# Kernel optimization log

Hardware: AMD Instinct MI355X
Metric: run time of the kernel (lower is better)

Reference implementation:

```python
import jax, jax.numpy as jnp
import numpy as np

# static config (matches torch module instantiation)
B, D, NH, HD = 2, 256, 8, 32
NL, NP, DFF = 1, 4, 1024
SHAPES = [(180, 180)]          # (H, W) per level; 180*180 = 32400
STARTS = [0]
LSRC = 32400
N_DET, N_SEG = 200, 100        # SEG_QUERY_NUM=100 -> num_seg_query=300
LQ = N_DET + N_SEG


def _lin(key, dout, din, scale=None):
    scale = scale if scale is not None else 1.0 / np.sqrt(din)
    k1, k2 = jax.random.split(key)
    return (jax.random.normal(k1, (dout, din), jnp.float32) * scale,
            jax.random.normal(k2, (dout,), jnp.float32) * 0.01)


def setup_inputs() -> dict:
    key = jax.random.key(0)
    ks = iter(jax.random.split(key, 64))
    inp = {
        'query': jax.random.normal(next(ks), (B, LQ, D), jnp.float32),
        'query_pos': jax.random.normal(next(ks), (B, LQ, D), jnp.float32),
        'src': jax.random.normal(next(ks), (B, LSRC, D), jnp.float32),
        'pos': jax.random.normal(next(ks), (B, LSRC, D), jnp.float32),
        'reference_points': jax.random.uniform(next(ks), (B, LSRC + LQ, NL, 2), jnp.float32),
        'spatial_shapes': jnp.array(SHAPES, jnp.int32),
        'level_start_index': jnp.array(STARTS, jnp.int32),
    }
    # two MSDeformAttn instances (self_attn = sa_*, cross_attn = ca_*)
    for pre in ('sa', 'ca'):
        inp[pre + '_Wv'], inp[pre + '_bv'] = _lin(next(ks), D, D)
        inp[pre + '_Woff'], inp[pre + '_boff'] = _lin(next(ks), NH * NL * NP * 2, D, scale=0.01)
        inp[pre + '_Waw'], inp[pre + '_baw'] = _lin(next(ks), NH * NL * NP, D, scale=0.01)
        inp[pre + '_Wout'], inp[pre + '_bout'] = _lin(next(ks), D, D)
    for nm in ('norm1', 'norm2', 'normq', 'qa_norm', 'norm3'):
        inp[nm + '_g'] = jnp.ones((D,), jnp.float32)
        inp[nm + '_b'] = jnp.zeros((D,), jnp.float32)
    inp['ffn1_W1'], inp['ffn1_b1'] = _lin(next(ks), DFF, D)
    inp['ffn1_W2'], inp['ffn1_b2'] = _lin(next(ks), D, DFF)
    inp['ffn3_W1'], inp['ffn3_b1'] = _lin(next(ks), DFF, D)
    inp['ffn3_W2'], inp['ffn3_b2'] = _lin(next(ks), D, DFF)
    # TCSLayer: proj(d->2d) then gate1/gate2 (d->d), sigmoid gates
    inp['tcs_Wp'], inp['tcs_bp'] = _lin(next(ks), 2 * D, D)
    inp['tcs_Wg1'], inp['tcs_bg1'] = _lin(next(ks), D, D)
    inp['tcs_Wg2'], inp['tcs_bg2'] = _lin(next(ks), D, D)
    # query self-attention (nn.MultiheadAttention): packed in_proj [3D, D]
    inp['qa_Win'], inp['qa_bin'] = _lin(next(ks), 3 * D, D)
    inp['qa_Wout'], inp['qa_bout'] = _lin(next(ks), D, D)
    return inp


def ln(x, g, b, eps=1e-5):
    m = x.mean(-1, keepdims=True)
    v = ((x - m) ** 2).mean(-1, keepdims=True)
    return (x - m) * jax.lax.rsqrt(v + eps) * g + b


def msda(q, ref, src_v, Wv, bv, Woff, boff, Waw, baw, Wout, bout):
    """MSDeformAttn: value proj -> learned offsets/weights -> bilinear sample -> out proj.
    q [B,Lq,D], ref [B,Lq,NL,2] in [0,1], src_v [B,Lin,D]."""
    Bq, Lq, _ = q.shape
    Lin = src_v.shape[1]
    value = (src_v @ Wv.T + bv).reshape(Bq, Lin, NH, HD).transpose(0, 2, 1, 3)  # [B,NH,Lin,HD]
    off = (q @ Woff.T + boff).reshape(Bq, Lq, NH, NL, NP, 2)
    aw = jax.nn.softmax((q @ Waw.T + baw).reshape(Bq, Lq, NH, NL * NP), -1)
    aw = aw.reshape(Bq, Lq, NH, NL, NP)
    norm = jnp.array([[w, h] for (h, w) in SHAPES], q.dtype)  # [NL,2] = (W,H)
    loc = ref[:, :, None, :, None, :] + off / norm[None, None, None, :, None, :]
    out = jnp.zeros((Bq, NH, Lq, HD), q.dtype)
    for l, (h, w) in enumerate(SHAPES):
        s = STARTS[l]
        v_l = value[:, :, s:s + h * w, :]
        # grid_sample align_corners=False: pixel = loc*size - 0.5, zero padding
        x = loc[:, :, :, l, :, 0] * w - 0.5  # [B,Lq,NH,NP]
        y = loc[:, :, :, l, :, 1] * h - 0.5
        x0 = jnp.floor(x); y0 = jnp.floor(y)
        lx = x - x0; ly = y - y0
        x0i = x0.astype(jnp.int32); y0i = y0.astype(jnp.int32)
        samp = jnp.zeros((Bq, NH, Lq, NP, HD), q.dtype)
        for dy, dx, wgt in ((0, 0, (1 - lx) * (1 - ly)), (0, 1, lx * (1 - ly)),
                            (1, 0, (1 - lx) * ly), (1, 1, lx * ly)):
            xi = x0i + dx; yi = y0i + dy
            valid = ((xi >= 0) & (xi < w) & (yi >= 0) & (yi < h)).astype(q.dtype)
            idx = jnp.clip(yi, 0, h - 1) * w + jnp.clip(xi, 0, w - 1)  # [B,Lq,NH,NP]
            idx_t = idx.transpose(0, 2, 1, 3).reshape(Bq, NH, Lq * NP)
            g = jnp.take_along_axis(v_l, idx_t[..., None], axis=2).reshape(Bq, NH, Lq, NP, HD)
            samp = samp + g * (wgt * valid).transpose(0, 2, 1, 3)[..., None]
        out = out + jnp.einsum('bhqpd,bqhp->bhqd', samp, aw[:, :, :, l, :])
    out = out.transpose(0, 2, 1, 3).reshape(Bq, Lq, NH * HD)
    return out @ Wout.T + bout


def mha(x, pos, Win, bin_, Wout, bout):
    qk = x + pos
    q = (qk @ Win[:D].T + bin_[:D]).reshape(*x.shape[:2], NH, HD)
    k = (qk @ Win[D:2 * D].T + bin_[D:2 * D]).reshape(*x.shape[:2], NH, HD)
    v = (x @ Win[2 * D:].T + bin_[2 * D:]).reshape(*x.shape[:2], NH, HD)
    attn = jax.nn.softmax(jnp.einsum('bqhd,bkhd->bhqk', q, k) / np.sqrt(HD), -1)
    o = jnp.einsum('bhqk,bkhd->bqhd', attn, v).reshape(*x.shape[:2], D)
    return o @ Wout.T + bout


def reference(query, query_pos, src, pos, reference_points, spatial_shapes, level_start_index,
              sa_Wv, sa_bv, sa_Woff, sa_boff, sa_Waw, sa_baw, sa_Wout, sa_bout,
              ca_Wv, ca_bv, ca_Woff, ca_boff, ca_Waw, ca_baw, ca_Wout, ca_bout,
              norm1_g, norm1_b, norm2_g, norm2_b, normq_g, normq_b,
              qa_norm_g, qa_norm_b, norm3_g, norm3_b,
              ffn1_W1, ffn1_b1, ffn1_W2, ffn1_b2,
              ffn3_W1, ffn3_b1, ffn3_W2, ffn3_b2,
              tcs_Wp, tcs_bp, tcs_Wg1, tcs_bg1, tcs_Wg2, tcs_bg2,
              qa_Win, qa_bin, qa_Wout, qa_bout):
    # deformable self-attn over BEV tokens
    src2 = msda(src + pos, reference_points[:, :LSRC], src,
                sa_Wv, sa_bv, sa_Woff, sa_boff, sa_Waw, sa_baw, sa_Wout, sa_bout)
    src = ln(src + src2, norm1_g, norm1_b)
    # FFN 1
    h = jax.nn.relu(src @ ffn1_W1.T + ffn1_b1) @ ffn1_W2.T + ffn1_b2
    src = ln(src + h, norm2_g, norm2_b)
    # TCS gating (USE_SIGMOID_GATE, not SPLIT_GATE, no OCC)
    gd, gs = jnp.split(jax.nn.gelu(src @ tcs_Wp.T + tcs_bp, approximate=False), 2, axis=-1)
    gate_det = jax.nn.sigmoid(gd @ tcs_Wg1.T + tcs_bg1)
    gate_seg = jax.nn.sigmoid(gs @ tcs_Wg2.T + tcs_bg2)
    # gated deformable cross-attn (shared cross_attn weights)
    q_det = msda(query[:, :N_DET] + query_pos[:, :N_DET],
                 reference_points[:, LSRC:LSRC + N_DET], src * gate_det,
                 ca_Wv, ca_bv, ca_Woff, ca_boff, ca_Waw, ca_baw, ca_Wout, ca_bout)
    q_seg = msda(query[:, N_DET:LQ] + query_pos[:, N_DET:LQ],
                 reference_points[:, LSRC + N_DET:LSRC + LQ], src * gate_seg,
                 ca_Wv, ca_bv, ca_Woff, ca_boff, ca_Waw, ca_baw, ca_Wout, ca_bout)
    query2 = jnp.concatenate([q_det, q_seg], 1)
    query = ln(query + query2, normq_g, normq_b)
    # query self-attention (post-norm)
    query = ln(query + mha(query, query_pos, qa_Win, qa_bin, qa_Wout, qa_bout),
               qa_norm_g, qa_norm_b)
    # FFN 3
    h3 = jax.nn.relu(query @ ffn3_W1.T + ffn3_b1) @ ffn3_W2.T + ffn3_b2
    query = ln(query + h3, norm3_g, norm3_b)
    return (query, src, gate_det, gate_seg)
```

## Files before the change

kernel.cpp:

```cpp
#include <hip/hip_runtime.h>
#include <hip/hip_bf16.h>
#include <cmath>

using bf16 = __hip_bfloat16;
typedef __bf16 bf16x8 __attribute__((ext_vector_type(8)));
typedef __bf16 bf16x4 __attribute__((ext_vector_type(4)));
typedef float f32x4 __attribute__((ext_vector_type(4)));

constexpr int D = 256;
constexpr int LSRC = 32400;
constexpr int NB = 2;
constexpr int LQ = 300;
constexpr int NDET = 200;
constexpr int MS = NB * LSRC;
constexpr int MQ = NB * LQ;
constexpr int RP_STRIDE = LSRC + LQ;
constexpr float IMGW = 180.f, IMGH = 180.f;
constexpr int IW = 180, IH = 180;

constexpr long long OFF_Q  = 0;
constexpr long long OFF_S  = (long long)MQ * D;
constexpr long long OFF_GD = OFF_S + (long long)MS * D;
constexpr long long OFF_GS = OFF_GD + (long long)MS * D;

__device__ inline void gload16(const void* g, void* l) {
  __builtin_amdgcn_global_load_lds(
      (const __attribute__((address_space(1))) void*)g,
      (__attribute__((address_space(3))) void*)l, 16, 0, 0);
}

__device__ inline int xcd_swz(int b, int nwg) {
  int q = nwg >> 3, r = nwg & 7;
  int xcd = b & 7, i = b >> 3;
  return (xcd < r ? xcd * (q + 1) : r * (q + 1) + (xcd - r) * q) + i;
}

__global__ void detect_kernel(const void* g, int* flag) {
  *flag = (*(const unsigned*)g == 0x3F803F80u) ? 1 : 0;
}

struct CvtEnt { const void* src; void* dst; int n; int f32out; };
struct CvtBatch { CvtEnt e[48]; int blk0[49]; int cnt; };

__global__ __launch_bounds__(256) void cvt_batch_kernel(CvtBatch cb, const int* __restrict__ flag) {
  int bid = blockIdx.x;
  int i = 0;
  for (int j = 1; j < cb.cnt; ++j) if (cb.blk0[j] <= bid) i = j;
  const CvtEnt en = cb.e[i];
  int idx = (bid - cb.blk0[i]) * 2048 + threadIdx.x * 8;
  if (idx >= en.n) return;
  const bool isb = (*flag != 0);
  if (en.f32out) {
    float v[8];
    if (isb) {
      bf16x8 x = *(const bf16x8*)((const __bf16*)en.src + idx);
#pragma unroll
      for (int j = 0; j < 8; ++j) v[j] = (float)x[j];
    } else {
      const float* s = (const float*)en.src + idx;
#pragma unroll
      for (int j = 0; j < 8; ++j) v[j] = s[j];
    }
    float* o = (float*)en.dst + idx;
#pragma unroll
    for (int j = 0; j < 8; ++j) o[j] = v[j];
  } else {
    if (isb) {
      uint4 x = *(const uint4*)((const char*)en.src + (size_t)idx * 2);
      *(uint4*)((char*)en.dst + (size_t)idx * 2) = x;
    } else {
      const float* s = (const float*)en.src + idx;
      bf16x8 o;
#pragma unroll
      for (int j = 0; j < 8; ++j) o[j] = (__bf16)s[j];
      *(bf16x8*)((__bf16*)en.dst + idx) = o;
    }
  }
}

__global__ __launch_bounds__(256) void cvt_add(const void* __restrict__ a, const void* __restrict__ b,
                                               const int* __restrict__ flag,
                                               bf16* __restrict__ a_b, bf16* __restrict__ b_b,
                                               bf16* __restrict__ sum, int n8) {
  int i = blockIdx.x * 256 + threadIdx.x;
  if (i >= n8) return;
  const bool isb = (*flag != 0);
  float va[8], vb[8];
  bf16x8 ab, bb;
  if (isb) {
    ab = *(const bf16x8*)((const __bf16*)a + (size_t)i * 8);
    bb = *(const bf16x8*)((const __bf16*)b + (size_t)i * 8);
#pragma unroll
    for (int j = 0; j < 8; ++j) { va[j] = (float)ab[j]; vb[j] = (float)bb[j]; }
  } else {
    const float* pa = (const float*)a + (size_t)i * 8;
    const float* pb = (const float*)b + (size_t)i * 8;
#pragma unroll
    for (int j = 0; j < 8; ++j) { va[j] = pa[j]; vb[j] = pb[j]; ab[j] = (__bf16)va[j]; bb[j] = (__bf16)vb[j]; }
  }
  bf16x8 sb;
#pragma unroll
  for (int j = 0; j < 8; ++j) sb[j] = (__bf16)(va[j] + vb[j]);
  if (a_b) *(bf16x8*)((__bf16*)a_b + (size_t)i * 8) = ab;
  if (b_b) *(bf16x8*)((__bf16*)b_b + (size_t)i * 8) = bb;
  *(bf16x8*)((__bf16*)sum + (size_t)i * 8) = sb;
}

__global__ __launch_bounds__(256) void add8(const bf16* __restrict__ a, const bf16* __restrict__ b,
                                            bf16* __restrict__ o, int n8) {
  int i = blockIdx.x * 256 + threadIdx.x;
  if (i >= n8) return;
  bf16x8 va = *(const bf16x8*)((const __bf16*)a + (size_t)i * 8);
  bf16x8 vb = *(const bf16x8*)((const __bf16*)b + (size_t)i * 8);
  bf16x8 vo;
#pragma unroll
  for (int j = 0; j < 8; ++j) vo[j] = (__bf16)((float)va[j] + (float)vb[j]);
  *(bf16x8*)((__bf16*)o + (size_t)i * 8) = vo;
}

template<int ACT, int OUTB, int RESM>
__global__ __launch_bounds__(256) void gemm_bt(
    const bf16* __restrict__ A, int lda,
    const bf16* __restrict__ Wt,
    const bf16* __restrict__ bias,
    const void* __restrict__ res,
    void* __restrict__ out, int ldo,
    int M, int N, int K)
{
  __shared__ __bf16 As[2][64 * 32];
  __shared__ __bf16 Bs[2][64 * 32];
  const int gy = gridDim.y;
  const int nwg = gridDim.x * gy;
  const int t = xcd_swz(blockIdx.y * gridDim.x + blockIdx.x, nwg);
  const int m0 = (t / gy) * 64;
  const int n0 = (t % gy) * 64;
  const int tid = threadIdx.x;
  const int lane = tid & 63, wid = tid >> 6;
  const int wm = (wid >> 1) * 32, wn = (wid & 1) * 32;
  f32x4 acc[2][2] = {};
  const int lr = tid >> 2;
  const int lc = (tid & 3) * 8;
  const bf16* Ap = A + (size_t)(m0 + lr) * lda + lc;
  const bf16* Wp = Wt + (size_t)(n0 + lr) * K + lc;
  const int fr = lane & 15, ks = (lane >> 4) * 8;

  for (int k0 = 0; k0 < K; k0 += 64) {
    __syncthreads();
#pragma unroll
    for (int kk = 0; kk < 2; ++kk) {
      const int kc = k0 + kk * 32;
      gload16((const __bf16*)Ap + kc, &As[kk][8 * tid]);
      gload16((const __bf16*)Wp + kc, &Bs[kk][8 * tid]);
    }
    __syncthreads();
#pragma unroll
    for (int kk = 0; kk < 2; ++kk) {
      bf16x8 a0 = *(const bf16x8*)&As[kk][(wm + fr) * 32 + ks];
      bf16x8 a1 = *(const bf16x8*)&As[kk][(wm + 16 + fr) * 32 + ks];
      bf16x8 b0 = *(const bf16x8*)&Bs[kk][(wn + fr) * 32 + ks];
      bf16x8 b1 = *(const bf16x8*)&Bs[kk][(wn + 16 + fr) * 32 + ks];
      acc[0][0] = __builtin_amdgcn_mfma_f32_16x16x32_bf16(a0, b0, acc[0][0], 0, 0, 0);
      acc[0][1] = __builtin_amdgcn_mfma_f32_16x16x32_bf16(a0, b1, acc[0][1], 0, 0, 0);
      acc[1][0] = __builtin_amdgcn_mfma_f32_16x16x32_bf16(a1, b0, acc[1][0], 0, 0, 0);
      acc[1][1] = __builtin_amdgcn_mfma_f32_16x16x32_bf16(a1, b1, acc[1][1], 0, 0, 0);
    }
  }

  const int rq = (lane >> 4) * 4;
#pragma unroll
  for (int fm = 0; fm < 2; ++fm)
#pragma unroll
  for (int fn = 0; fn < 2; ++fn) {
    int ncol = n0 + wn + fn * 16 + fr;
    if (ncol >= N) continue;
    float bvs = (float)bias[ncol];
#pragma unroll
    for (int i = 0; i < 4; ++i) {
      int mrow = m0 + wm + fm * 16 + rq + i;
      if (mrow >= M) continue;
      float v = acc[fm][fn][i] + bvs;
      if (RESM == 1) v += (float)((const bf16*)res)[(size_t)mrow * ldo + ncol];
      else if (RESM == 2) v += ((const float*)res)[(size_t)mrow * ldo + ncol];
      if (ACT == 1) v = fmaxf(v, 0.f);
      else if (ACT == 2) v = 0.5f * v * (1.f + erff(v * 0.7071067811865476f));
      else if (ACT == 3) v = 1.f / (1.f + __expf(-v));
      if (OUTB) ((bf16*)out)[(size_t)mrow * ldo + ncol] = (bf16)v;
      else ((float*)out)[(size_t)mrow * ldo + ncol] = v;
    }
  }
}

template<int ACT, int OUTB, int RESM, int EMIT>
__global__ __launch_bounds__(256) void gemm128(
    const bf16* __restrict__ A, int lda,
    const bf16* __restrict__ Wt,
    const bf16* __restrict__ bias,
    const void* __restrict__ res,
    void* __restrict__ out, int ldo,
    int M, int N, int K,
    const int* __restrict__ flagp, void* __restrict__ ob, long long eoff)
{
  __shared__ __bf16 As[2][128 * 32];
  __shared__ __bf16 Bs[2][128 * 32];
  const int gy = gridDim.y;
  const int nwg = gridDim.x * gy;
  const int t = xcd_swz(blockIdx.y * gridDim.x + blockIdx.x, nwg);
  const int m0 = (t / gy) * 128;
  const int n0 = (t % gy) * 128;
  const int tid = threadIdx.x;
  const int lane = tid & 63, wid = tid >> 6;
  const int wr = (wid >> 1) * 64, wc = (wid & 1) * 64;
  const int fr = lane & 15, ks = (lane >> 4) * 8;
  f32x4 acc[4][4] = {};

  const int srow = tid >> 2;
  const int scol = (tid & 3) * 8;
  const bf16* Ap0 = A + (size_t)(m0 + srow) * lda + scol;
  const bf16* Ap1 = A + (size_t)(m0 + 64 + srow) * lda + scol;
  const bf16* Bp0 = Wt + (size_t)(n0 + srow) * K + scol;
  const bf16* Bp1 = Wt + (size_t)(n0 + 64 + srow) * K + scol;

  for (int k0 = 0; k0 < K; k0 += 64) {
    __syncthreads();
#pragma unroll
    for (int kk = 0; kk < 2; ++kk) {
      const int kc = k0 + kk * 32;
      gload16((const __bf16*)Ap0 + kc, &As[kk][8 * tid]);
      gload16((const __bf16*)Ap1 + kc, &As[kk][64 * 32 + 8 * tid]);
      gload16((const __bf16*)Bp0 + kc, &Bs[kk][8 * tid]);
      gload16((const __bf16*)Bp1 + kc, &Bs[kk][64 * 32 + 8 * tid]);
    }
    __syncthreads();
#pragma unroll
    for (int kk = 0; kk < 2; ++kk) {
      bf16x8 af[4], bfv[4];
#pragma unroll
      for (int m = 0; m < 4; ++m) af[m]  = *(const bf16x8*)&As[kk][(wr + m * 16 + fr) * 32 + ks];
#pragma unroll
      for (int n = 0; n < 4; ++n) bfv[n] = *(const bf16x8*)&Bs[kk][(wc + n * 16 + fr) * 32 + ks];
#pragma unroll
      for (int m = 0; m < 4; ++m)
#pragma unroll
        for (int n = 0; n < 4; ++n)
          acc[m][n] = __builtin_amdgcn_mfma_f32_16x16x32_bf16(af[m], bfv[n], acc[m][n], 0, 0, 0);
    }
  }

  const bool isb = EMIT ? (*flagp != 0) : false;
  const int rq = (lane >> 4) * 4;
#pragma unroll
  for (int m = 0; m < 4; ++m) {
    const int mb = m0 + wr + m * 16 + rq;
#pragma unroll
    for (int n = 0; n < 4; ++n) {
      const int ncol = n0 + wc + n * 16 + fr;
      const float bvs = (float)bias[ncol];
#pragma unroll
      for (int i = 0; i < 4; ++i) {
        const int mrow = mb + i;
        if (mrow >= M) continue;
        float v = acc[m][n][i] + bvs;
        if (RESM == 1) v += (float)((const bf16*)res)[(size_t)mrow * ldo + ncol];
        else if (RESM == 2) v += ((const float*)res)[(size_t)mrow * ldo + ncol];
        if (ACT == 1) v = fmaxf(v, 0.f);
        else if (ACT == 2) v = 0.5f * v * (1.f + erff(v * 0.7071067811865476f));
        else if (ACT == 3) v = 1.f / (1.f + __expf(-v));
        if (OUTB) ((bf16*)out)[(size_t)mrow * ldo + ncol] = (bf16)v;
        else ((float*)out)[(size_t)mrow * ldo + ncol] = v;
        if (EMIT) {
          long long eo = eoff + (long long)mrow * ldo + ncol;
          if (isb) ((__bf16*)ob)[eo] = (__bf16)v;
          else ((float*)ob)[eo] = v;
        }
      }
    }
  }
}

__global__ __launch_bounds__(256) void gemm_gated(
    const bf16* __restrict__ S, const bf16* __restrict__ G, int lda,
    const bf16* __restrict__ Wt,
    const bf16* __restrict__ bias,
    bf16* __restrict__ out, int ldo,
    int M, int N, int K)
{
  __shared__ __bf16 As[2][128 * 32];
  __shared__ __bf16 Bs[2][128 * 32];
  const int gy = gridDim.y;
  const int nwg = gridDim.x * gy;
  const int t = xcd_swz(blockIdx.y * gridDim.x + blockIdx.x, nwg);
  const int m0 = (t / gy) * 128;
  const int n0 = (t % gy) * 128;
  const int tid = threadIdx.x;
  const int lane = tid & 63, wid = tid >> 6;
  const int wr = (wid >> 1) * 64, wc = (wid & 1) * 64;
  const int fr = lane & 15, ks = (lane >> 4) * 8;
  f32x4 acc[4][4] = {};

  const int srow = tid >> 2;
  const int scol = (tid & 3) * 8;
  const bf16* Sp0 = S + (size_t)(m0 + srow) * lda + scol;
  const bf16* Sp1 = S + (size_t)(m0 + 64 + srow) * lda + scol;
  const bf16* Gp0 = G + (size_t)(m0 + srow) * lda + scol;
  const bf16* Gp1 = G + (size_t)(m0 + 64 + srow) * lda + scol;
  const bf16* Bp0 = Wt + (size_t)(n0 + srow) * K + scol;
  const bf16* Bp1 = Wt + (size_t)(n0 + 64 + srow) * K + scol;

  for (int k0 = 0; k0 < K; k0 += 64) {
    bf16x8 a0[2], a1[2];
#pragma unroll
    for (int kk = 0; kk < 2; ++kk) {
      const int kc = k0 + kk * 32;
      bf16x8 s0 = *(const bf16x8*)((const __bf16*)Sp0 + kc);
      bf16x8 g0 = *(const bf16x8*)((const __bf16*)Gp0 + kc);
      bf16x8 s1 = *(const bf16x8*)((const __bf16*)Sp1 + kc);
      bf16x8 g1 = *(const bf16x8*)((const __bf16*)Gp1 + kc);
#pragma unroll
      for (int j = 0; j < 8; ++j) {
        a0[kk][j] = (__bf16)((float)s0[j] * (float)g0[j]);
        a1[kk][j] = (__bf16)((float)s1[j] * (float)g1[j]);
      }
    }
    __syncthreads();
#pragma unroll
    for (int kk = 0; kk < 2; ++kk) {
      const int kc = k0 + kk * 32;
      *(bf16x8*)&As[kk][8 * tid] = a0[kk];
      *(bf16x8*)&As[kk][64 * 32 + 8 * tid] = a1[kk];
      gload16((const __bf16*)Bp0 + kc, &Bs[kk][8 * tid]);
      gload16((const __bf16*)Bp1 + kc, &Bs[kk][64 * 32 + 8 * tid]);
    }
    __syncthreads();
#pragma unroll
    for (int kk = 0; kk < 2; ++kk) {
      bf16x8 af[4], bfv[4];
#pragma unroll
      for (int m = 0; m < 4; ++m) af[m]  = *(const bf16x8*)&As[kk][(wr + m * 16 + fr) * 32 + ks];
#pragma unroll
      for (int n = 0; n < 4; ++n) bfv[n] = *(const bf16x8*)&Bs[kk][(wc + n * 16 + fr) * 32 + ks];
#pragma unroll
      for (int m = 0; m < 4; ++m)
#pragma unroll
        for (int n = 0; n < 4; ++n)
          acc[m][n] = __builtin_amdgcn_mfma_f32_16x16x32_bf16(af[m], bfv[n], acc[m][n], 0, 0, 0);
    }
  }

  const int rq = (lane >> 4) * 4;
#pragma unroll
  for (int m = 0; m < 4; ++m) {
    const int mb = m0 + wr + m * 16 + rq;
#pragma unroll
    for (int n = 0; n < 4; ++n) {
      const int ncol = n0 + wc + n * 16 + fr;
      const float bvs = (float)bias[ncol];
#pragma unroll
      for (int i = 0; i < 4; ++i) {
        const int mrow = mb + i;
        if (mrow >= M) continue;
        out[(size_t)mrow * ldo + ncol] = (bf16)(acc[m][n][i] + bvs);
      }
    }
  }
}

template<int RESM, int EMIT, int OUTF>
__global__ __launch_bounds__(256) void gemm_ln(
    const bf16* __restrict__ A, int lda,
    const bf16* __restrict__ Wt,
    const bf16* __restrict__ bias,
    const void* __restrict__ res,
    const bf16* __restrict__ g, const bf16* __restrict__ b,
    bf16* __restrict__ outb, float* __restrict__ outf,
    int M, int K,
    const int* __restrict__ flagp, void* __restrict__ ob, long long eoff)
{
  __shared__ __bf16 As[2][64 * 32];
  __shared__ __bf16 Bs[2][256 * 32];
  __shared__ float redS[4][64], redQ[4][64];
  const int m0 = blockIdx.x * 64;
  const int tid = threadIdx.x, lane = tid & 63, wid = tid >> 6;
  const int wc = wid * 64;
  const int fr = lane & 15, ks = (lane >> 4) * 8;
  f32x4 acc[4][4] = {};
  const int srow = tid >> 2, scol = (tid & 3) * 8;
  const bf16* Ap = A + (size_t)(m0 + srow) * lda + scol;
  const bf16* Bp = Wt + (size_t)srow * K + scol;

  for (int k0 = 0; k0 < K; k0 += 64) {
    __syncthreads();
#pragma unroll
    for (int kk = 0; kk < 2; ++kk) {
      const int kc = k0 + kk * 32;
      gload16((const __bf16*)Ap + kc, &As[kk][8 * tid]);
#pragma unroll
      for (int j = 0; j < 4; ++j)
        gload16((const __bf16*)(Bp + (size_t)j * 64 * K) + kc, &Bs[kk][j * 64 * 32 + 8 * tid]);
    }
    __syncthreads();
#pragma unroll
    for (int kk = 0; kk < 2; ++kk) {
      bf16x8 af[4], bfv[4];
#pragma unroll
      for (int m = 0; m < 4; ++m) af[m]  = *(const bf16x8*)&As[kk][(m * 16 + fr) * 32 + ks];
#pragma unroll
      for (int n = 0; n < 4; ++n) bfv[n] = *(const bf16x8*)&Bs[kk][(wc + n * 16 + fr) * 32 + ks];
#pragma unroll
      for (int m = 0; m < 4; ++m)
#pragma unroll
        for (int n = 0; n < 4; ++n)
          acc[m][n] = __builtin_amdgcn_mfma_f32_16x16x32_bf16(af[m], bfv[n], acc[m][n], 0, 0, 0);
    }
  }

  const int rq = (lane >> 4) * 4;
  float bvals[4], gvals[4], bb2[4];
#pragma unroll
  for (int n = 0; n < 4; ++n) {
    bvals[n] = (float)bias[wc + n * 16 + fr];
    gvals[n] = (float)g[wc + n * 16 + fr];
    bb2[n]   = (float)b[wc + n * 16 + fr];
  }
#pragma unroll
  for (int m = 0; m < 4; ++m)
#pragma unroll
  for (int i = 0; i < 4; ++i) {
    const int mrow = m0 + m * 16 + rq + i;
#pragma unroll
    for (int n = 0; n < 4; ++n) {
      float r;
      if (RESM == 1) r = (float)((const bf16*)res)[(size_t)mrow * 256 + wc + n * 16 + fr];
      else           r = ((const float*)res)[(size_t)mrow * 256 + wc + n * 16 + fr];
      acc[m][n][i] += bvals[n] + r;
    }
    float s = acc[m][0][i] + acc[m][1][i] + acc[m][2][i] + acc[m][3][i];
    float q = acc[m][0][i] * acc[m][0][i] + acc[m][1][i] * acc[m][1][i]
            + acc[m][2][i] * acc[m][2][i] + acc[m][3][i] * acc[m][3][i];
#pragma unroll
    for (int off = 1; off <= 8; off <<= 1) {
      s += __shfl_xor(s, off);
      q += __shfl_xor(q, off);
    }
    if (fr == 0) { redS[wid][m * 16 + rq + i] = s; redQ[wid][m * 16 + rq + i] = q; }
  }
  __syncthreads();
  const bool isb = EMIT ? (*flagp != 0) : false;
#pragma unroll
  for (int m = 0; m < 4; ++m)
#pragma unroll
  for (int i = 0; i < 4; ++i) {
    const int rl = m * 16 + rq + i;
    const int mrow = m0 + rl;
    if (mrow >= M) continue;
    float ts = redS[0][rl] + redS[1][rl] + redS[2][rl] + redS[3][rl];
    float tq = redQ[0][rl] + redQ[1][rl] + redQ[2][rl] + redQ[3][rl];
    float mean = ts * (1.f / 256.f);
    float var = tq * (1.f / 256.f) - mean * mean;
    float rstd = rsqrtf(var + 1e-5f);
#pragma unroll
    for (int n = 0; n < 4; ++n) {
      const int col = wc + n * 16 + fr;
      float y = (acc[m][n][i] - mean) * rstd * gvals[n] + bb2[n];
      if (outb) outb[(size_t)mrow * 256 + col] = (bf16)y;
      if (OUTF) outf[(size_t)mrow * 256 + col] = y;
      if (EMIT) {
        long long eo = eoff + (long long)mrow * 256 + col;
        if (isb) ((__bf16*)ob)[eo] = (__bf16)y;
        else ((float*)ob)[eo] = y;
      }
    }
  }
}

__global__ __launch_bounds__(256) void msda_sample4(
    const float* __restrict__ oa,
    const float* __restrict__ rpf, int rp_base, int qi0, int qcnt4, int lqrow,
    const bf16* __restrict__ val, bf16* __restrict__ out) {
  int blk = blockIdx.x;
  int b = blk / qcnt4;
  int wid = threadIdx.x >> 6, lane = threadIdx.x & 63;
  int qi = qi0 + (blk % qcnt4) * 4 + wid;
  size_t row = (size_t)b * lqrow + qi;
  int h = lane >> 3, d0 = (lane & 7) * 4;
  const __bf16* vb = (const __bf16*)val + (size_t)b * LSRC * 256 + h * 32 + d0;
  float rx = rpf[((size_t)b * RP_STRIDE + rp_base + qi) * 2 + 0];
  float ry = rpf[((size_t)b * RP_STRIDE + rp_base + qi) * 2 + 1];
  const float* offp = oa + row * 96 + h * 8;
  const float* awp  = oa + row * 96 + 64 + h * 4;
  float a0 = awp[0], a1 = awp[1], a2 = awp[2], a3 = awp[3];
  float mx = fmaxf(fmaxf(a0, a1), fmaxf(a2, a3));
  float e0 = __expf(a0 - mx), e1 = __expf(a1 - mx), e2 = __expf(a2 - mx), e3 = __expf(a3 - mx);
  float rs = 1.f / (e0 + e1 + e2 + e3);
  float aws[4] = { e0 * rs, e1 * rs, e2 * rs, e3 * rs };
  float o0 = 0.f, o1 = 0.f, o2 = 0.f, o3 = 0.f;
#pragma unroll
  for (int p = 0; p < 4; ++p) {
    float x = rx * IMGW + offp[p * 2 + 0] - 0.5f;
    float y = ry * IMGH + offp[p * 2 + 1] - 0.5f;
    float x0f = floorf(x), y0f = floorf(y);
    float lx = x - x0f, ly = y - y0f;
    int x0 = (int)x0f, y0 = (int)y0f;
#pragma unroll
    for (int dy = 0; dy < 2; ++dy)
#pragma unroll
    for (int dx = 0; dx < 2; ++dx) {
      int xi = x0 + dx, yi = y0 + dy;
      if (xi >= 0 && xi < IW && yi >= 0 && yi < IH) {
        float wgt = aws[p] * (dx ? lx : 1.f - lx) * (dy ? ly : 1.f - ly);
        bf16x4 gv = *(const bf16x4*)(vb + (size_t)(yi * IW + xi) * 256);
        o0 += wgt * (float)gv[0]; o1 += wgt * (float)gv[1];
        o2 += wgt * (float)gv[2]; o3 += wgt * (float)gv[3];
      }
    }
  }
  bf16x4 ov;
  ov[0] = (__bf16)o0; ov[1] = (__bf16)o1; ov[2] = (__bf16)o2; ov[3] = (__bf16)o3;
  *(bf16x4*)((__bf16*)out + row * 256 + h * 32 + d0) = ov;
}

__global__ __launch_bounds__(256) void mha_attn(
    const float* __restrict__ qk,
    const float* __restrict__ v,
    bf16* __restrict__ o) {
  __shared__ float probs[4][304];
  int bh = blockIdx.x / 75;
  int j  = blockIdx.x % 75;
  int b = bh >> 3, h = bh & 7;
  int wid = threadIdx.x >> 6, lane = threadIdx.x & 63;
  const float scale = 0.17677669529663687f;
  int q = j * 4 + wid;
  const float* qv = qk + ((size_t)(b * 300 + q)) * 512 + h * 32;
  float p[5];
  float mx = -1e30f;
#pragma unroll
  for (int s5 = 0; s5 < 5; ++s5) {
    int k = lane + 64 * s5;
    float sacc = -1e30f;
    if (k < 300) {
      const float* kv = qk + ((size_t)(b * 300 + k)) * 512 + 256 + h * 32;
      float sd = 0.f;
#pragma unroll
      for (int dd = 0; dd < 32; ++dd) sd += qv[dd] * kv[dd];
      sacc = sd * scale;
    }
    p[s5] = sacc;
    mx = fmaxf(mx, sacc);
  }
#pragma unroll
  for (int off = 32; off; off >>= 1) mx = fmaxf(mx, __shfl_xor(mx, off));
  float ssum = 0.f;
#pragma unroll
  for (int s5 = 0; s5 < 5; ++s5) {
    p[s5] = (p[s5] > -1e29f) ? __expf(p[s5] - mx) : 0.f;
    ssum += p[s5];
  }
#pragma unroll
  for (int off = 32; off; off >>= 1) ssum += __shfl_xor(ssum, off);
  float rinv = 1.f / ssum;
#pragma unroll
  for (int s5 = 0; s5 < 5; ++s5) {
    int k = lane + 64 * s5;
    if (k < 300) probs[wid][k] = p[s5] * rinv;
  }
  __syncthreads();
  {
    int d = lane & 31, half = lane >> 5;
    float acc = 0.f;
    for (int k = half * 150; k < half * 150 + 150; ++k)
      acc += probs[wid][k] * v[((size_t)(b * 300 + k)) * 256 + h * 32 + d];
    acc += __shfl_xor(acc, 32);
    if (lane < 32) o[((size_t)(b * 300 + q)) * 256 + h * 32 + d] = (bf16)acc;
  }
}

extern "C" void kernel_launch(void* const* d_in, const int* in_sizes, int n_in,
                              void* d_out, int out_size, void* d_ws, size_t ws_size,
                              hipStream_t stream) {
  (void)n_in; (void)out_size; (void)ws_size;
  const size_t SZ = (size_t)MS * D * sizeof(bf16);

  char* w = (char*)d_ws;
  auto carve = [&](size_t bytes) { char* p = w; w += (bytes + 255) & ~(size_t)255; return p; };

  int*   flag = (int*)carve(256);
  float* rp_f = (float*)carve((size_t)NB * RP_STRIDE * 2 * 4);

  bf16* wb[51] = {};
  bf16* wcat_s = nullptr; bf16* bcat_s = nullptr;
  bf16* wcat_q = nullptr; bf16* bcat_q = nullptr;
  for (int i = 7; i <= 50; ++i) {
    if (i == 9)       { wcat_s = (bf16*)carve((size_t)96 * 256 * 2); wb[9]  = wcat_s; }
    else if (i == 10) { bcat_s = (bf16*)carve(96 * 2);               wb[10] = bcat_s; }
    else if (i == 11) { wb[11] = wcat_s + 64 * 256; }
    else if (i == 12) { wb[12] = bcat_s + 64; }
    else if (i == 17) { wcat_q = (bf16*)carve((size_t)96 * 256 * 2); wb[17] = wcat_q; }
    else if (i == 18) { bcat_q = (bf16*)carve(96 * 2);               wb[18] = bcat_q; }
    else if (i == 19) { wb[19] = wcat_q + 64 * 256; }
    else if (i == 20) { wb[20] = bcat_q + 64; }
    else wb[i] = (bf16*)carve((size_t)in_sizes[i] * 2);
  }

  bf16* query_b     = (bf16*)carve((size_t)MQ * D * 2);
  bf16* query_pos_b = (bf16*)carve((size_t)MQ * D * 2);
  bf16* qx_q        = (bf16*)carve((size_t)MQ * D * 2);
  bf16* att_q       = (bf16*)carve((size_t)MQ * D * 2);
  bf16* q_x         = (bf16*)carve((size_t)MQ * D * 2);
  bf16* qpx         = (bf16*)carve((size_t)MQ * D * 2);
  bf16* mha_o       = (bf16*)carve((size_t)MQ * D * 2);
  bf16* lnq_b       = (bf16*)carve((size_t)MQ * D * 2);
  bf16* qh          = (bf16*)carve((size_t)MQ * 1024 * 2);
  float* qoffawb    = (float*)carve((size_t)MQ * 96 * 4);
  float* q_res      = (float*)carve((size_t)MQ * D * 4);
  float* qk_f       = (float*)carve((size_t)MQ * 512 * 4);
  float* v_f        = (float*)carve((size_t)MQ * D * 4);

  char* A = carve(SZ);
  char* B = carve(SZ);
  char* C = carve(SZ);
  char* Dd = carve(SZ);
  char* E = carve(SZ);
  carve(512 * 1024);

  const bf16* query     = (const bf16*)d_in[0];
  const bf16* query_pos = (const bf16*)d_in[1];
  const bf16* src       = (const bf16*)d_in[2];
  const bf16* pos       = (const bf16*)d_in[3];

  dim3 blk(256);
  const int GS64  = (MS + 63) / 64;
  const int GQ64  = (MQ + 63) / 64;
  const int G128  = (MS + 127) / 128;
  const int G128h = (MS / 2 + 127) / 128;

  detect_kernel<<<1, 1, 0, stream>>>(d_in[23], flag);
  {
    CvtBatch cb{};
    int nb = 0, cnt = 0;
    auto addcvt = [&](const void* s, void* dst, int n, int f32o) {
      cb.e[cnt] = { s, dst, n, f32o };
      cb.blk0[cnt] = nb;
      nb += (n + 2047) / 2048;
      ++cnt;
    };
    addcvt(d_in[4], rp_f, in_sizes[4], 1);
    for (int i = 7; i <= 50; ++i) addcvt(d_in[i], wb[i], in_sizes[i], 0);
    cb.cnt = cnt;
    cvt_batch_kernel<<<nb, blk, 0, stream>>>(cb, flag);
  }
  bf16* src_b = (bf16*)A;
  bf16* qx    = (bf16*)C;
  cvt_add<<<MS * D / 8 / 256, blk, 0, stream>>>(src, pos, flag, src_b, nullptr, qx, MS * D / 8);
  cvt_add<<<MQ * D / 8 / 256, blk, 0, stream>>>(query, query_pos, flag, query_b, query_pos_b, qx_q, MQ * D / 8);

  float* offawb = (float*)B;
  bf16*  val    = (bf16*)Dd;
  gemm_bt<0,0,0><<<dim3(GS64,2), blk, 0, stream>>>(qx, 256, wb[9], wb[10], nullptr, offawb, 96, MS, 96, 256);
  gemm128<0,1,0,0><<<dim3(G128,2), blk, 0, stream>>>(src_b, 256, wb[7], wb[8], nullptr, val, 256, MS, 256, 256, nullptr, nullptr, 0);
  bf16* samp = (bf16*)C;
  msda_sample4<<<NB * (LSRC / 4), blk, 0, stream>>>(offawb, rp_f, 0, 0, LSRC / 4, LSRC, val, samp);
  bf16* lnx = (bf16*)C;
  gemm_ln<1,0,0><<<GS64, blk, 0, stream>>>(samp, 256, wb[13], wb[14], src_b, wb[23], wb[24],
                                           lnx, nullptr, MS, 256, nullptr, nullptr, 0);

  bf16* srcout = (bf16*)A;
  {
    const int CH = MS / 2;
    const int GC128 = (CH + 127) / 128;
    const int GC64  = (CH + 63) / 64;
    bf16* hid = (bf16*)Dd;
    for (int c = 0; c < 2; ++c) {
      size_t ro = (size_t)c * CH * 256;
      gemm128<1,1,0,0><<<dim3(GC128,8), blk, 0, stream>>>(lnx + ro, 256, wb[33], wb[34], nullptr, hid, 1024, CH, 1024, 256, nullptr, nullptr, 0);
      gemm_ln<1,1,0><<<GC64, blk, 0, stream>>>(hid, 1024, wb[35], wb[36], lnx + ro, wb[25], wb[26],
                                               srcout + ro, nullptr, CH, 1024, flag, d_out, OFF_S + (long long)ro);
    }
  }

  bf16* gdt = (bf16*)B;
  bf16* gst = (bf16*)E;
  {
    const int CH = MS / 2;
    bf16* proj = (bf16*)C;
    for (int c = 0; c < 2; ++c) {
      size_t ro = (size_t)c * CH * 256;
      gemm128<2,1,0,0><<<dim3(G128h,4), blk, 0, stream>>>(srcout + ro, 256, wb[41], wb[42], nullptr, proj, 512, CH, 512, 256, nullptr, nullptr, 0);
      gemm128<3,1,0,1><<<dim3(G128h,2), blk, 0, stream>>>(proj,       512, wb[43], wb[44], nullptr, gdt + ro, 256, CH, 256, 256, flag, d_out, OFF_GD + (long long)ro);
      gemm128<3,1,0,1><<<dim3(G128h,2), blk, 0, stream>>>(proj + 256, 512, wb[45], wb[46], nullptr, gst + ro, 256, CH, 256, 256, flag, d_out, OFF_GS + (long long)ro);
    }
  }

  gemm_bt<0,0,0><<<dim3(GQ64,2), blk, 0, stream>>>(qx_q, 256, wb[17], wb[18], nullptr, qoffawb, 96, MQ, 96, 256);

  gemm_gated<<<dim3(G128,2), blk, 0, stream>>>(srcout, gdt, 256, wb[15], wb[16], val, 256, MS, 256, 256);
  msda_sample4<<<NB * (NDET / 4), blk, 0, stream>>>(qoffawb, rp_f, LSRC, 0, NDET / 4, LQ, val, att_q);
  gemm_gated<<<dim3(G128,2), blk, 0, stream>>>(srcout, gst, 256, wb[15], wb[16], val, 256, MS, 256, 256);
  msda_sample4<<<NB * ((LQ - NDET) / 4), blk, 0, stream>>>(qoffawb, rp_f, LSRC, NDET, (LQ - NDET) / 4, LQ, val, att_q);

  gemm_ln<1,0,1><<<GQ64, blk, 0, stream>>>(att_q, 256, wb[21], wb[22], query_b, wb[27], wb[28],
                                           q_x, q_res, MQ, 256, nullptr, nullptr, 0);

  add8<<<MQ * D / 8 / 256, blk, 0, stream>>>(q_x, query_pos_b, qpx, MQ * D / 8);
  gemm_bt<0,0,0><<<dim3(GQ64,8), blk, 0, stream>>>(qpx, 256, wb[47], wb[48], nullptr, qk_f, 512, MQ, 512, 256);
  gemm_bt<0,0,0><<<dim3(GQ64,4), blk, 0, stream>>>(q_x, 256, wb[47] + (size_t)512 * 256, wb[48] + 512, nullptr, v_f, 256, MQ, 256, 256);
  mha_attn<<<NB * 8 * 75, blk, 0, stream>>>(qk_f, v_f, mha_o);
  gemm_ln<2,0,1><<<GQ64, blk, 0, stream>>>(mha_o, 256, wb[49], wb[50], q_res, wb[29], wb[30],
                                           q_x, q_res, MQ, 256, nullptr, nullptr, 0);

  gemm_bt<1,1,0><<<dim3(GQ64,16), blk, 0, stream>>>(q_x, 256, wb[37], wb[38], nullptr, qh, 1024, MQ, 1024, 256);
  gemm_ln<2,1,0><<<GQ64, blk, 0, stream>>>(qh, 1024, wb[39], wb[40], q_res, wb[31], wb[32],
                                           lnq_b, nullptr, MQ, 1024, flag, d_out, OFF_Q);
}
```

Before: 756.3 us.

## Fuse two-layer MLPs and gate GEMMs into single back-to-back GEMM kernels

Adds a gemm2_fused kernel that computes the first GEMM with its activation into shared memory, then feeds that hidden tile straight into the second GEMM with a residual+LayerNorm or sigmoid epilogue. It replaces the src FFN, the TCS proj+gate pairs and the query FFN, so the large hidden and proj buffers no longer make a global-memory round trip. It also enables an XCD block swizzle on the big sampling kernel. The cost is that projection GEMMs are recomputed per gate branch and each block uses only 64-row tiles, which lowers MFMA reuse and occupancy because of the larger shared-memory footprint.

Measured after the change: 798.0 us. 5.5% more time.

```diff
diff --git a/kernel.cpp b/kernel.cpp
--- a/kernel.cpp
+++ b/kernel.cpp
@@ -472,11 +472,195 @@
   }
 }
 
+template<int NCH, int ACT1, int EPI, int RESM, int EMIT, int OUTF>
+__global__ __launch_bounds__(256) void gemm2_fused(
+    const bf16* __restrict__ A,
+    const bf16* __restrict__ W1,
+    const bf16* __restrict__ b1,
+    const bf16* __restrict__ W2,
+    const bf16* __restrict__ b2,
+    const void* __restrict__ res,
+    const bf16* __restrict__ g, const bf16* __restrict__ b,
+    bf16* __restrict__ outb, float* __restrict__ outf,
+    int M,
+    const int* __restrict__ flagp, void* __restrict__ ob, long long eoff)
+{
+  constexpr int K1 = 256;
+  constexpr int N1 = NCH * 256;
+  __shared__ __bf16 As[2][64 * 32];
+  __shared__ __bf16 Bs[2][256 * 32];
+  __shared__ __bf16 Hs[8][64 * 32];
+  __shared__ float redS[4][64], redQ[4][64];
+  const int m0 = blockIdx.x * 64;
+  const int tid = threadIdx.x, lane = tid & 63, wid = tid >> 6;
+  const int wc = wid * 64;
+  const int fr = lane & 15, ks = (lane >> 4) * 8;
+  const int rq = (lane >> 4) * 4;
+  const int srow = tid >> 2, scol = (tid & 3) * 8;
+  const bf16* Ap = A + (size_t)(m0 + srow) * K1 + scol;
+
+  f32x4 acc2[4][4] = {};
+
+  for (int nch = 0; nch < NCH; ++nch) {
+    f32x4 acc1[4][4] = {};
+    const bf16* B1p = W1 + (size_t)(nch * 256 + srow) * K1 + scol;
+    for (int k0 = 0; k0 < K1; k0 += 64) {
+      __syncthreads();
+#pragma unroll
+      for (int kk = 0; kk < 2; ++kk) {
+        const int kc = k0 + kk * 32;
+        gload16((const __bf16*)Ap + kc, &As[kk][8 * tid]);
+#pragma unroll
+        for (int j = 0; j < 4; ++j)
+          gload16((const __bf16*)(B1p + (size_t)j * 64 * K1) + kc, &Bs[kk][j * 64 * 32 + 8 * tid]);
+      }
+      __syncthreads();
+#pragma unroll
+      for (int kk = 0; kk < 2; ++kk) {
+        bf16x8 af[4], bfv[4];
+#pragma unroll
+        for (int m = 0; m < 4; ++m) af[m]  = *(const bf16x8*)&As[kk][(m * 16 + fr) * 32 + ks];
+#pragma unroll
+        for (int n = 0; n < 4; ++n) bfv[n] = *(const bf16x8*)&Bs[kk][(wc + n * 16 + fr) * 32 + ks];
+#pragma unroll
+        for (int m = 0; m < 4; ++m)
+#pragma unroll
+          for (int n = 0; n < 4; ++n)
+            acc1[m][n] = __builtin_amdgcn_mfma_f32_16x16x32_bf16(af[m], bfv[n], acc1[m][n], 0, 0, 0);
+      }
+    }
+#pragma unroll
+    for (int n = 0; n < 4; ++n) {
+      const int c = wc + n * 16 + fr;
+      const float bv = (float)b1[nch * 256 + c];
+      const int kb = c >> 5, kcol = c & 31;
+#pragma unroll
+      for (int m = 0; m < 4; ++m)
+#pragma unroll
+      for (int i = 0; i < 4; ++i) {
+        float v = acc1[m][n][i] + bv;
+        if (ACT1 == 1) v = fmaxf(v, 0.f);
+        else if (ACT1 == 2) v = 0.5f * v * (1.f + erff(v * 0.7071067811865476f));
+        Hs[kb][(m * 16 + rq + i) * 32 + kcol] = (__bf16)v;
+      }
+    }
+    const bf16* B2p = W2 + (size_t)srow * N1 + nch * 256 + scol;
+    for (int k0 = 0; k0 < 256; k0 += 64) {
+      __syncthreads();
+#pragma unroll
+      for (int kk = 0; kk < 2; ++kk) {
+        const int kc = k0 + kk * 32;
+#pragma unroll
+        for (int j = 0; j < 4; ++j)
+          gload16((const __bf16*)(B2p + (size_t)j * 64 * N1) + kc, &Bs[kk][j * 64 * 32 + 8 * tid]);
+      }
+      __syncthreads();
+#pragma unroll
+      for (int kk = 0; kk < 2; ++kk) {
+        const int kb = (k0 >> 5) + kk;
+        bf16x8 af[4], bfv[4];
+#pragma unroll
+        for (int m = 0; m < 4; ++m) af[m]  = *(const bf16x8*)&Hs[kb][(m * 16 + fr) * 32 + ks];
+#pragma unroll
+        for (int n = 0; n < 4; ++n) bfv[n] = *(const bf16x8*)&Bs[kk][(wc + n * 16 + fr) * 32 + ks];
+#pragma unroll
+        for (int m = 0; m < 4; ++m)
+#pragma unroll
+          for (int n = 0; n < 4; ++n)
+            acc2[m][n] = __builtin_amdgcn_mfma_f32_16x16x32_bf16(af[m], bfv[n], acc2[m][n], 0, 0, 0);
+      }
+    }
+  }
+
+  float bvals[4];
+#pragma unroll
+  for (int n = 0; n < 4; ++n) bvals[n] = (float)b2[wc + n * 16 + fr];
+  const bool isb = EMIT ? (*flagp != 0) : false;
+
+  if (EPI == 1) {
+#pragma unroll
+    for (int m = 0; m < 4; ++m)
+#pragma unroll
+    for (int n = 0; n < 4; ++n) {
+      const int col = wc + n * 16 + fr;
+#pragma unroll
+      for (int i = 0; i < 4; ++i) {
+        const int mrow = m0 + m * 16 + rq + i;
+        if (mrow >= M) continue;
+        float v = 1.f / (1.f + __expf(-(acc2[m][n][i] + bvals[n])));
+        outb[(size_t)mrow * 256 + col] = (bf16)v;
+        if (EMIT) {
+          long long eo = eoff + (long long)mrow * 256 + col;
+          if (isb) ((__bf16*)ob)[eo] = (__bf16)v;
+          else ((float*)ob)[eo] = v;
+        }
+      }
+    }
+    return;
+  }
+
+  float gvals[4], bb2[4];
+#pragma unroll
+  for (int n = 0; n < 4; ++n) {
+    gvals[n] = (float)g[wc + n * 16 + fr];
+    bb2[n]   = (float)b[wc + n * 16 + fr];
+  }
+#pragma unroll
+  for (int m = 0; m < 4; ++m)
+#pragma unroll
+  for (int i = 0; i < 4; ++i) {
+    const int mrow = m0 + m * 16 + rq + i;
+#pragma unroll
+    for (int n = 0; n < 4; ++n) {
+      float r;
+      if (RESM == 1) r = (float)((const bf16*)res)[(size_t)mrow * 256 + wc + n * 16 + fr];
+      else           r = ((const float*)res)[(size_t)mrow * 256 + wc + n * 16 + fr];
+      acc2[m][n][i] += bvals[n] + r;
+    }
+    float s = acc2[m][0][i] + acc2[m][1][i] + acc2[m][2][i] + acc2[m][3][i];
+    float q = acc2[m][0][i] * acc2[m][0][i] + acc2[m][1][i] * acc2[m][1][i]
+            + acc2[m][2][i] * acc2[m][2][i] + acc2[m][3][i] * acc2[m][3][i];
+#pragma unroll
+    for (int off = 1; off <= 8; off <<= 1) {
+      s += __shfl_xor(s, off);
+      q += __shfl_xor(q, off);
+    }
+    if (fr == 0) { redS[wid][m * 16 + rq + i] = s; redQ[wid][m * 16 + rq + i] = q; }
+  }
+  __syncthreads();
+#pragma unroll
+  for (int m = 0; m < 4; ++m)
+#pragma unroll
+  for (int i = 0; i < 4; ++i) {
+    const int rl = m * 16 + rq + i;
+    const int mrow = m0 + rl;
+    if (mrow >= M) continue;
+    float ts = redS[0][rl] + redS[1][rl] + redS[2][rl] + redS[3][rl];
+    float tq = redQ[0][rl] + redQ[1][rl] + redQ[2][rl] + redQ[3][rl];
+    float mean = ts * (1.f / 256.f);
+    float var = tq * (1.f / 256.f) - mean * mean;
+    float rstd = rsqrtf(var + 1e-5f);
+#pragma unroll
+    for (int n = 0; n < 4; ++n) {
+      const int col = wc + n * 16 + fr;
+      float y = (acc2[m][n][i] - mean) * rstd * gvals[n] + bb2[n];
+      if (outb) outb[(size_t)mrow * 256 + col] = (bf16)y;
+      if (OUTF) outf[(size_t)mrow * 256 + col] = y;
+      if (EMIT) {
+        long long eo = eoff + (long long)mrow * 256 + col;
+        if (isb) ((__bf16*)ob)[eo] = (__bf16)y;
+        else ((float*)ob)[eo] = y;
+      }
+    }
+  }
+}
+
 __global__ __launch_bounds__(256) void msda_sample4(
     const float* __restrict__ oa,
     const float* __restrict__ rpf, int rp_base, int qi0, int qcnt4, int lqrow,
-    const bf16* __restrict__ val, bf16* __restrict__ out) {
+    const bf16* __restrict__ val, bf16* __restrict__ out, int swz) {
   int blk = blockIdx.x;
+  if (swz) blk = xcd_swz(blk, gridDim.x);
   int b = blk / qcnt4;
   int wid = threadIdx.x >> 6, lane = threadIdx.x & 63;
   int qi = qi0 + (blk % qcnt4) * 4 + wid;
@@ -608,7 +792,6 @@
   bf16* qpx         = (bf16*)carve((size_t)MQ * D * 2);
   bf16* mha_o       = (bf16*)carve((size_t)MQ * D * 2);
   bf16* lnq_b       = (bf16*)carve((size_t)MQ * D * 2);
-  bf16* qh          = (bf16*)carve((size_t)MQ * 1024 * 2);
   float* qoffawb    = (float*)carve((size_t)MQ * 96 * 4);
   float* q_res      = (float*)carve((size_t)MQ * D * 4);
   float* qk_f       = (float*)carve((size_t)MQ * 512 * 4);
@@ -627,10 +810,9 @@
   const bf16* pos       = (const bf16*)d_in[3];
 
   dim3 blk(256);
-  const int GS64  = (MS + 63) / 64;
-  const int GQ64  = (MQ + 63) / 64;
-  const int G128  = (MS + 127) / 128;
-  const int G128h = (MS / 2 + 127) / 128;
+  const int GS64 = (MS + 63) / 64;
+  const int GQ64 = (MQ + 63) / 64;
+  const int G128 = (MS + 127) / 128;
 
   detect_kernel<<<1, 1, 0, stream>>>(d_in[23], flag);
   {
@@ -657,44 +839,31 @@
   gemm_bt<0,0,0><<<dim3(GS64,2), blk, 0, stream>>>(qx, 256, wb[9], wb[10], nullptr, offawb, 96, MS, 96, 256);
   gemm128<0,1,0,0><<<dim3(G128,2), blk, 0, stream>>>(src_b, 256, wb[7], wb[8], nullptr, val, 256, MS, 256, 256, nullptr, nullptr, 0);
   bf16* samp = (bf16*)C;
-  msda_sample4<<<NB * (LSRC / 4), blk, 0, stream>>>(offawb, rp_f, 0, 0, LSRC / 4, LSRC, val, samp);
+  msda_sample4<<<NB * (LSRC / 4), blk, 0, stream>>>(offawb, rp_f, 0, 0, LSRC / 4, LSRC, val, samp, 1);
   bf16* lnx = (bf16*)C;
   gemm_ln<1,0,0><<<GS64, blk, 0, stream>>>(samp, 256, wb[13], wb[14], src_b, wb[23], wb[24],
                                            lnx, nullptr, MS, 256, nullptr, nullptr, 0);
 
   bf16* srcout = (bf16*)A;
-  {
-    const int CH = MS / 2;
-    const int GC128 = (CH + 127) / 128;
-    const int GC64  = (CH + 63) / 64;
-    bf16* hid = (bf16*)Dd;
-    for (int c = 0; c < 2; ++c) {
-      size_t ro = (size_t)c * CH * 256;
-      gemm128<1,1,0,0><<<dim3(GC128,8), blk, 0, stream>>>(lnx + ro, 256, wb[33], wb[34], nullptr, hid, 1024, CH, 1024, 256, nullptr, nullptr, 0);
-      gemm_ln<1,1,0><<<GC64, blk, 0, stream>>>(hid, 1024, wb[35], wb[36], lnx + ro, wb[25], wb[26],
-                                               srcout + ro, nullptr, CH, 1024, flag, d_out, OFF_S + (long long)ro);
-    }
-  }
+  gemm2_fused<4,1,0,1,1,0><<<GS64, blk, 0, stream>>>(
+      lnx, wb[33], wb[34], wb[35], wb[36], lnx, wb[25], wb[26],
+      srcout, nullptr, MS, flag, d_out, OFF_S);
 
   bf16* gdt = (bf16*)B;
   bf16* gst = (bf16*)E;
-  {
-    const int CH = MS / 2;
-    bf16* proj = (bf16*)C;
-    for (int c = 0; c < 2; ++c) {
-      size_t ro = (size_t)c * CH * 256;
-      gemm128<2,1,0,0><<<dim3(G128h,4), blk, 0, stream>>>(srcout + ro, 256, wb[41], wb[42], nullptr, proj, 512, CH, 512, 256, nullptr, nullptr, 0);
-      gemm128<3,1,0,1><<<dim3(G128h,2), blk, 0, stream>>>(proj,       512, wb[43], wb[44], nullptr, gdt + ro, 256, CH, 256, 256, flag, d_out, OFF_GD + (long long)ro);
-      gemm128<3,1,0,1><<<dim3(G128h,2), blk, 0, stream>>>(proj + 256, 512, wb[45], wb[46], nullptr, gst + ro, 256, CH, 256, 256, flag, d_out, OFF_GS + (long long)ro);
-    }
-  }
+  gemm2_fused<1,2,1,0,1,0><<<GS64, blk, 0, stream>>>(
+      srcout, wb[41], wb[42], wb[43], wb[44], nullptr, nullptr, nullptr,
+      gdt, nullptr, MS, flag, d_out, OFF_GD);
+  gemm2_fused<1,2,1,0,1,0><<<GS64, blk, 0, stream>>>(
+      srcout, wb[41] + (size_t)256 * 256, wb[42] + 256, wb[45], wb[46], nullptr, nullptr, nullptr,
+      gst, nullptr, MS, flag, d_out, OFF_GS);
 
   gemm_bt<0,0,0><<<dim3(GQ64,2), blk, 0, stream>>>(qx_q, 256, wb[17], wb[18], nullptr, qoffawb, 96, MQ, 96, 256);
 
   gemm_gated<<<dim3(G128,2), blk, 0, stream>>>(srcout, gdt, 256, wb[15], wb[16], val, 256, MS, 256, 256);
-  msda_sample4<<<NB * (NDET / 4), blk, 0, stream>>>(qoffawb, rp_f, LSRC, 0, NDET / 4, LQ, val, att_q);
+  msda_sample4<<<NB * (NDET / 4), blk, 0, stream>>>(qoffawb, rp_f, LSRC, 0, NDET / 4, LQ, val, att_q, 0);
   gemm_gated<<<dim3(G128,2), blk, 0, stream>>>(srcout, gst, 256, wb[15], wb[16], val, 256, MS, 256, 256);
-  msda_sample4<<<NB * ((LQ - NDET) / 4), blk, 0, stream>>>(qoffawb, rp_f, LSRC, NDET, (LQ - NDET) / 4, LQ, val, att_q);
+  msda_sample4<<<NB * ((LQ - NDET) / 4), blk, 0, stream>>>(qoffawb, rp_f, LSRC, NDET, (LQ - NDET) / 4, LQ, val, att_q, 0);
 
   gemm_ln<1,0,1><<<GQ64, blk, 0, stream>>>(att_q, 256, wb[21], wb[22], query_b, wb[27], wb[28],
                                            q_x, q_res, MQ, 256, nullptr, nullptr, 0);
@@ -706,7 +875,7 @@
   gemm_ln<2,0,1><<<GQ64, blk, 0, stream>>>(mha_o, 256, wb[49], wb[50], q_res, wb[29], wb[30],
                                            q_x, q_res, MQ, 256, nullptr, nullptr, 0);
 
-  gemm_bt<1,1,0><<<dim3(GQ64,16), blk, 0, stream>>>(q_x, 256, wb[37], wb[38], nullptr, qh, 1024, MQ, 1024, 256);
-  gemm_ln<2,1,0><<<GQ64, blk, 0, stream>>>(qh, 1024, wb[39], wb[40], q_res, wb[31], wb[32],
-                                           lnq_b, nullptr, MQ, 1024, flag, d_out, OFF_Q);
-}
+  gemm2_fused<4,1,0,2,1,0><<<GQ64, blk, 0, stream>>>(
+      q_x, wb[37], wb[38], wb[39], wb[40], q_res, wb[31], wb[32],
+      lnq_b, nullptr, MQ, flag, d_out, OFF_Q);
+}
```
